# Optimization experiments

Measured on AMD Instinct MI355X. Metric: run time of the kernel, lower is better.

The kernel has to match this reference:

```python
import jax, jax.numpy as jnp
import numpy as np

IMAGE_SIZE = 224  # self.image_size; dims are all equal to this so postprocess is one bilinear resize
EPS = 1e-12      # F.normalize default eps


def setup_inputs() -> dict:
    key = jax.random.key(0)
    k1, k2 = jax.random.split(key)
    embeddings = jax.random.normal(k1, (2, 9, 256, 48, 48), dtype=jnp.float32)
    # binary class masks in {0,1}; channel 0 (background) is recomputed inside forward
    prompt_masks = jax.random.randint(k2, (2, 8, 4, 48, 48), 0, 2).astype(jnp.float32)
    dims = jnp.full((2, 1, 2), IMAGE_SIZE, dtype=jnp.int32)  # all original sizes == image_size
    return {"embeddings": embeddings, "prompt_masks": prompt_masks, "dims": dims}


def reference(embeddings, prompt_masks, dims):
    B, M, D, H, W = embeddings.shape
    HW = H * W
    q = embeddings[:, 0]            # (B, D, H, W)  query
    s = embeddings[:, 1:]           # (B, M-1, D, H, W)  supports
    # F.normalize: x / max(||x||, eps) along the feature dim
    qn = q / jnp.maximum(jnp.sqrt(jnp.sum(q * q, axis=1, keepdims=True)), EPS)
    sn = s / jnp.maximum(jnp.sqrt(jnp.sum(s * s, axis=2, keepdims=True)), EPS)

    q2 = qn.reshape(B, D, HW).transpose(0, 2, 1)              # (B, Q, D)
    s2 = sn.reshape(B, M - 1, D, HW).transpose(0, 1, 3, 2)    # (B, M1, K, D)
    sim = jnp.einsum('bqd,bmkd->bqmk', q2, s2)                # (B, Q, M1, K) cosine sims

    # nearest-resize of prompt masks to compare_size==(H,W) is identity here (same size)
    N = prompt_masks.shape[2]
    pm = prompt_masks.reshape(B, M - 1, N, HW)
    background = (pm[:, :, 1:, :].sum(axis=2) == 0).astype(sim.dtype)  # (B, M1, HW)
    pm = pm.at[:, :, 0, :].set(background)

    neg_inf = jnp.array(-jnp.inf, sim.dtype)
    logits = []
    for n in range(N):  # small fixed class count
        cm = pm[:, :, n, :][:, None]                 # (B, 1, M1, K) broadcast over Q
        masked = jnp.where(cm == 0, neg_inf, sim)    # (B, Q, M1, K)
        logits.append(masked.reshape(B, HW, -1).max(axis=-1))  # (B, Q)
    logits = jnp.stack(logits, axis=1).reshape(B, N, H, W)

    # postprocess_masks: bilinear to image_size; all original sizes == image_size so the
    # per-image second interpolate is identity and padding amounts are zero.
    out = jax.image.resize(logits, (B, N, IMAGE_SIZE, IMAGE_SIZE), method='bilinear')
    # masks[:,0][masks[:,0]==-inf] = 0  (no-op here, kept for faithfulness)
    out = out.at[:, 0].set(jnp.where(jnp.isneginf(out[:, 0]), 0.0, out[:, 0]))
    return out
```

## Files before the change

### kernel.cpp

```cpp
#include <hip/hip_runtime.h>
#include <hip/hip_bf16.h>
#include <math.h>

#define BB 2
#define MM 9
#define MS 8
#define DD 256
#define HW 2304
#define NCLS 4
#define OUTR 224

typedef float floatx4 __attribute__((ext_vector_type(4)));
typedef __bf16 bf16x8 __attribute__((ext_vector_type(8)));
typedef unsigned short ushortx8 __attribute__((ext_vector_type(8)));

__device__ __forceinline__ unsigned enc_f(float f) {
    unsigned u = __float_as_uint(f);
    return (u & 0x80000000u) ? ~u : (u | 0x80000000u);
}
__device__ __forceinline__ float dec_f(unsigned k) {
    unsigned u = (k & 0x80000000u) ? (k & 0x7FFFFFFFu) : ~k;
    return __uint_as_float(u);
}

__global__ __launch_bounds__(256) void knorm(const float* __restrict__ emb,
                                             __hip_bfloat16* __restrict__ outp,
                                             unsigned* __restrict__ enc_logits) {
    __shared__ float tile[256][33];
    __shared__ float psum[8][32];
    __shared__ float sscale[32];
    const int bm   = blockIdx.y;
    const int pix0 = blockIdx.x * 32;
    const int tid  = threadIdx.x;

    int flat = (blockIdx.y * gridDim.x + blockIdx.x) * 256 + tid;
    if (flat < BB * NCLS * HW) enc_logits[flat] = 0u;

    const float* src = emb + (size_t)bm * DD * HW + pix0;
    {
        const int dr = tid >> 3;
        const int p4 = (tid & 7) * 4;
#pragma unroll
        for (int r = 0; r < 8; ++r) {
            int d = r * 32 + dr;
            floatx4 v = *(const floatx4*)(src + (size_t)d * HW + p4);
            float* t = &tile[d][p4];
            t[0] = v[0]; t[1] = v[1]; t[2] = v[2]; t[3] = v[3];
        }
    }
    __syncthreads();
    {
        const int pc = tid & 31;
        const int dr = tid >> 5;
        float ss = 0.f;
#pragma unroll
        for (int s = 0; s < 32; ++s) {
            float v = tile[dr * 32 + s][pc];
            ss += v * v;
        }
        psum[dr][pc] = ss;
    }
    __syncthreads();
    if (tid < 32) {
        float t = 0.f;
#pragma unroll
        for (int c = 0; c < 8; ++c) t += psum[c][tid];
        sscale[tid] = 1.0f / fmaxf(sqrtf(t), 1e-12f);
    }
    __syncthreads();
    unsigned* dstu = (unsigned*)(outp + (size_t)bm * HW * DD + (size_t)pix0 * DD);
    const int d2 = tid & 127;
    const int ph = tid >> 7;
#pragma unroll
    for (int it = 0; it < 16; ++it) {
        int p = it * 2 + ph;
        float sc = sscale[p];
        float v0 = tile[2 * d2][p] * sc;
        float v1 = tile[2 * d2 + 1][p] * sc;
        unsigned pack = ((unsigned)__bfloat16_as_ushort(__float2bfloat16(v1)) << 16) |
                        (unsigned)__bfloat16_as_ushort(__float2bfloat16(v0));
        dstu[(size_t)p * 128 + d2] = pack;
    }
}

__device__ __forceinline__ void gld16(const unsigned short* g, unsigned short* l) {
    __builtin_amdgcn_global_load_lds((__attribute__((address_space(1))) void*)g,
                                     (__attribute__((address_space(3))) void*)l, 16, 0, 0);
}

#define BK 32
#define REDSTRIDE 132
#define SMEM_BYTES 33792

__global__ __launch_bounds__(256, 4) void kgemm(const unsigned short* __restrict__ normed,
                                                const float* __restrict__ pm,
                                                unsigned* __restrict__ enc_logits) {
    __shared__ __attribute__((aligned(16))) unsigned char smem[SMEM_BYTES];
    unsigned short* const S0 = (unsigned short*)smem;
    float* red = (float*)smem;

    const int ct = blockIdx.x;
    const int rt = blockIdx.y;
    const int b  = blockIdx.z;
    const int m  = ct / 18;
    const int kt = ct % 18;

    const int tid  = threadIdx.x;
    const int lane = tid & 63;
    const int wave = tid >> 6;
    const int wr = wave >> 1, wc = wave & 1;
    const int lrow = lane & 15;
    const int quad = lane >> 4;

    const unsigned short* A  = normed + (size_t)(b * MM) * (HW * DD) + (size_t)(rt * 128) * DD;
    const unsigned short* Bp = normed + (size_t)(b * MM + 1 + m) * (HW * DD) + (size_t)(kt * 128) * DD;

    const float* pmB = pm + (size_t)(b * MS + m) * NCLS * HW;
    int mj[4];
#pragma unroll
    for (int j = 0; j < 4; ++j) {
        int kp = kt * 128 + wc * 64 + j * 16 + lrow;
        float p1 = pmB[HW + kp], p2 = pmB[2 * HW + kp], p3 = pmB[3 * HW + kp];
        mj[j] = ((p1 + p2 + p3 == 0.0f) ? 1 : 0) | (p1 != 0.0f ? 2 : 0) |
                (p2 != 0.0f ? 4 : 0) | (p3 != 0.0f ? 8 : 0);
    }

    const int srq  = lane >> 2;
    const int scol = ((lane & 3) ^ ((srq >> 1) & 3)) * 8;
    const unsigned short* gA = A  + (size_t)(wave * 32 + srq) * DD + scol;
    const unsigned short* gB = Bp + (size_t)(wave * 32 + srq) * DD + scol;

    floatx4 zero = {0.f, 0.f, 0.f, 0.f};
    floatx4 acc[4][4];
#pragma unroll
    for (int i = 0; i < 4; ++i)
#pragma unroll
        for (int j = 0; j < 4; ++j) acc[i][j] = zero;

#pragma unroll
    for (int q = 0; q < 2; ++q) {
        gld16(gA + (size_t)(q * 16) * DD, S0 +        (wave * 2 + q) * 512);
        gld16(gB + (size_t)(q * 16) * DD, S0 + 4096 + (wave * 2 + q) * 512);
    }
    __syncthreads();

    const int pc8 = (quad ^ ((lrow >> 1) & 3)) * 8;

#pragma unroll
    for (int t = 0; t < DD / BK; ++t) {
        const int cb = t & 1;
        unsigned short* const Ac = S0 + cb * 8192;
        unsigned short* const Bc = Ac + 4096;
        if (t < DD / BK - 1) {
            unsigned short* const An = S0 + (cb ^ 1) * 8192;
#pragma unroll
            for (int q = 0; q < 2; ++q) {
                gld16(gA + (size_t)(q * 16) * DD + (t + 1) * BK, An +        (wave * 2 + q) * 512);
                gld16(gB + (size_t)(q * 16) * DD + (t + 1) * BK, An + 4096 + (wave * 2 + q) * 512);
            }
        }
        bf16x8 af[4], bfr[4];
#pragma unroll
        for (int i = 0; i < 4; ++i) {
            int ar = wr * 64 + i * 16 + lrow;
            int br = wc * 64 + i * 16 + lrow;
            af[i]  = __builtin_bit_cast(bf16x8, *(const ushortx8*)(Ac + ar * 32 + pc8));
            bfr[i] = __builtin_bit_cast(bf16x8, *(const ushortx8*)(Bc + br * 32 + pc8));
        }
#pragma unroll
        for (int i = 0; i < 4; ++i)
#pragma unroll
            for (int j = 0; j < 4; ++j)
                acc[i][j] = __builtin_amdgcn_mfma_f32_16x16x32_bf16(af[i], bfr[j], acc[i][j], 0, 0, 0);
        __syncthreads();
    }

    const int col32 = wc * 16 + lrow;

#pragma unroll
    for (int p = 0; p < 2; ++p) {
        if (p) __syncthreads();
        bool bit[2][4];
#pragma unroll
        for (int nn = 0; nn < 2; ++nn) {
            int n = p * 2 + nn;
#pragma unroll
            for (int j = 0; j < 4; ++j) bit[nn][j] = (mj[j] >> n) & 1;
        }
#pragma unroll
        for (int nn = 0; nn < 2; ++nn) {
#pragma unroll
            for (int i = 0; i < 4; ++i) {
                floatx4 o;
#pragma unroll
                for (int r = 0; r < 4; ++r) {
                    float t0 = bit[nn][0] ? acc[i][0][r] : -INFINITY;
                    float t1 = bit[nn][1] ? acc[i][1][r] : -INFINITY;
                    float t2 = bit[nn][2] ? acc[i][2][r] : -INFINITY;
                    float t3 = bit[nn][3] ? acc[i][3][r] : -INFINITY;
                    o[r] = fmaxf(fmaxf(t0, t1), fmaxf(t2, t3));
                }
                int rowbase = wr * 64 + i * 16 + quad * 4;
                *(floatx4*)(red + ((size_t)(nn * 32 + col32)) * REDSTRIDE + rowbase) = o;
            }
        }
        __syncthreads();
        {
            int nn  = tid >> 7;
            int row = tid & 127;
            float v = -INFINITY;
#pragma unroll
            for (int c = 0; c < 32; ++c)
                v = fmaxf(v, red[((size_t)(nn * 32 + c)) * REDSTRIDE + row]);
            int n = p * 2 + nn;
            atomicMax(enc_logits + ((size_t)b * NCLS + n) * HW + rt * 128 + row, enc_f(v));
        }
    }
}

__global__ __launch_bounds__(256) void kresize(const unsigned* __restrict__ enc_logits,
                                               float* __restrict__ out) {
    int idx = blockIdx.x * 256 + threadIdx.x;
    if (idx >= BB * NCLS * OUTR * OUTR) return;
    int ox = idx % OUTR;
    int oy = (idx / OUTR) % OUTR;
    int bn = idx / (OUTR * OUTR);
    const unsigned* src = enc_logits + (size_t)bn * HW;
    const float inv = 48.0f / 224.0f;
    float sx = (ox + 0.5f) * inv - 0.5f;
    float sy = (oy + 0.5f) * inv - 0.5f;
    int x0 = (int)floorf(sx); float fx = sx - x0;
    int y0 = (int)floorf(sy); float fy = sy - y0;
    int x0c = min(max(x0, 0), 47), x1c = min(max(x0 + 1, 0), 47);
    int y0c = min(max(y0, 0), 47), y1c = min(max(y0 + 1, 0), 47);
    float v00 = dec_f(src[y0c * 48 + x0c]), v01 = dec_f(src[y0c * 48 + x1c]);
    float v10 = dec_f(src[y1c * 48 + x0c]), v11 = dec_f(src[y1c * 48 + x1c]);
    float v = (1.f - fy) * ((1.f - fx) * v00 + fx * v01) + fy * ((1.f - fx) * v10 + fx * v11);
    if ((bn & 3) == 0 && v == -INFINITY) v = 0.f;
    out[idx] = v;
}

extern "C" void kernel_launch(void* const* d_in, const int* in_sizes, int n_in,
                              void* d_out, int out_size, void* d_ws, size_t ws_size,
                              hipStream_t stream) {
    const float* emb = (const float*)d_in[0];
    const float* pm  = (const float*)d_in[1];
    float* out = (float*)d_out;

    char* ws = (char*)d_ws;
    const size_t normed_bytes = (size_t)BB * MM * HW * DD * 2;
    __hip_bfloat16* normed = (__hip_bfloat16*)(ws);
    unsigned*       enc    = (unsigned*)(ws + normed_bytes);

    knorm<<<dim3(HW / 32, BB * MM), 256, 0, stream>>>(emb, normed, enc);
    kgemm<<<dim3(144, 18, BB), 256, 0, stream>>>((const unsigned short*)normed, pm, enc);
    kresize<<<(BB * NCLS * OUTR * OUTR + 255) / 256, 256, 0, stream>>>(enc, out);
}
```

Before: 144.3 us.

## Replace atomicMax logit reduction with per-tile partials and a separate reduction kernel

The GEMM kernel previously combined per-column-tile maxima with encoded-float atomicMax into a zero-initialised buffer. Each column tile now writes its own partial maxima to a workspace slab, and a new reduction kernel takes the max over the 144 tiles before the resize. This removes atomic contention, the order-preserving encode/decode and the init done in the norm kernel. In exchange it adds about 10 MB of partial writes and reads plus an extra kernel launch.

```diff
diff --git a/kernel.cpp b/kernel.cpp
--- a/kernel.cpp
+++ b/kernel.cpp
@@ -9,32 +9,20 @@
 #define HW 2304
 #define NCLS 4
 #define OUTR 224
+#define NCT 144
 
 typedef float floatx4 __attribute__((ext_vector_type(4)));
 typedef __bf16 bf16x8 __attribute__((ext_vector_type(8)));
 typedef unsigned short ushortx8 __attribute__((ext_vector_type(8)));
 
-__device__ __forceinline__ unsigned enc_f(float f) {
-    unsigned u = __float_as_uint(f);
-    return (u & 0x80000000u) ? ~u : (u | 0x80000000u);
-}
-__device__ __forceinline__ float dec_f(unsigned k) {
-    unsigned u = (k & 0x80000000u) ? (k & 0x7FFFFFFFu) : ~k;
-    return __uint_as_float(u);
-}
-
 __global__ __launch_bounds__(256) void knorm(const float* __restrict__ emb,
-                                             __hip_bfloat16* __restrict__ outp,
-                                             unsigned* __restrict__ enc_logits) {
+                                             __hip_bfloat16* __restrict__ outp) {
     __shared__ float tile[256][33];
     __shared__ float psum[8][32];
     __shared__ float sscale[32];
     const int bm   = blockIdx.y;
     const int pix0 = blockIdx.x * 32;
     const int tid  = threadIdx.x;
-
-    int flat = (blockIdx.y * gridDim.x + blockIdx.x) * 256 + tid;
-    if (flat < BB * NCLS * HW) enc_logits[flat] = 0u;
 
     const float* src = emb + (size_t)bm * DD * HW + pix0;
     {
@@ -94,7 +82,7 @@
 
 __global__ __launch_bounds__(256, 4) void kgemm(const unsigned short* __restrict__ normed,
                                                 const float* __restrict__ pm,
-                                                unsigned* __restrict__ enc_logits) {
+                                                float* __restrict__ partial) {
     __shared__ __attribute__((aligned(16))) unsigned char smem[SMEM_BYTES];
     unsigned short* const S0 = (unsigned short*)smem;
     float* red = (float*)smem;
@@ -213,19 +201,32 @@
             for (int c = 0; c < 32; ++c)
                 v = fmaxf(v, red[((size_t)(nn * 32 + c)) * REDSTRIDE + row]);
             int n = p * 2 + nn;
-            atomicMax(enc_logits + ((size_t)b * NCLS + n) * HW + rt * 128 + row, enc_f(v));
-        }
-    }
-}
-
-__global__ __launch_bounds__(256) void kresize(const unsigned* __restrict__ enc_logits,
+            partial[((size_t)ct * BB + b) * (NCLS * HW) + (size_t)n * HW + rt * 128 + row] = v;
+        }
+    }
+}
+
+__global__ __launch_bounds__(256) void kred(const float* __restrict__ partial,
+                                            float* __restrict__ logits) {
+    int idx = blockIdx.x * 256 + threadIdx.x;
+    int b    = idx / (NCLS * HW);
+    int rest = idx % (NCLS * HW);
+    const float* p = partial + (size_t)b * (NCLS * HW) + rest;
+    float v = -INFINITY;
+#pragma unroll 8
+    for (int ct = 0; ct < NCT; ++ct)
+        v = fmaxf(v, p[(size_t)ct * (BB * NCLS * HW)]);
+    logits[idx] = v;
+}
+
+__global__ __launch_bounds__(256) void kresize(const float* __restrict__ logits,
                                                float* __restrict__ out) {
     int idx = blockIdx.x * 256 + threadIdx.x;
     if (idx >= BB * NCLS * OUTR * OUTR) return;
     int ox = idx % OUTR;
     int oy = (idx / OUTR) % OUTR;
     int bn = idx / (OUTR * OUTR);
-    const unsigned* src = enc_logits + (size_t)bn * HW;
+    const float* src = logits + (size_t)bn * HW;
     const float inv = 48.0f / 224.0f;
     float sx = (ox + 0.5f) * inv - 0.5f;
     float sy = (oy + 0.5f) * inv - 0.5f;
@@ -233,8 +234,8 @@
     int y0 = (int)floorf(sy); float fy = sy - y0;
     int x0c = min(max(x0, 0), 47), x1c = min(max(x0 + 1, 0), 47);
     int y0c = min(max(y0, 0), 47), y1c = min(max(y0 + 1, 0), 47);
-    float v00 = dec_f(src[y0c * 48 + x0c]), v01 = dec_f(src[y0c * 48 + x1c]);
-    float v10 = dec_f(src[y1c * 48 + x0c]), v11 = dec_f(src[y1c * 48 + x1c]);
+    float v00 = src[y0c * 48 + x0c], v01 = src[y0c * 48 + x1c];
+    float v10 = src[y1c * 48 + x0c], v11 = src[y1c * 48 + x1c];
     float v = (1.f - fy) * ((1.f - fx) * v00 + fx * v01) + fy * ((1.f - fx) * v10 + fx * v11);
     if ((bn & 3) == 0 && v == -INFINITY) v = 0.f;
     out[idx] = v;
@@ -248,11 +249,14 @@
     float* out = (float*)d_out;
 
     char* ws = (char*)d_ws;
-    const size_t normed_bytes = (size_t)BB * MM * HW * DD * 2;
-    __hip_bfloat16* normed = (__hip_bfloat16*)(ws);
-    unsigned*       enc    = (unsigned*)(ws + normed_bytes);
-
-    knorm<<<dim3(HW / 32, BB * MM), 256, 0, stream>>>(emb, normed, enc);
-    kgemm<<<dim3(144, 18, BB), 256, 0, stream>>>((const unsigned short*)normed, pm, enc);
-    kresize<<<(BB * NCLS * OUTR * OUTR + 255) / 256, 256, 0, stream>>>(enc, out);
-}
+    const size_t normed_bytes  = (size_t)BB * MM * HW * DD * 2;
+    const size_t partial_bytes = (size_t)NCT * BB * NCLS * HW * 4;
+    __hip_bfloat16* normed  = (__hip_bfloat16*)(ws);
+    float*          partial = (float*)(ws + normed_bytes);
+    float*          logits  = (float*)(ws + normed_bytes + partial_bytes);
+
+    knorm<<<dim3(HW / 32, BB * MM), 256, 0, stream>>>(emb, normed);
+    kgemm<<<dim3(NCT, 18, BB), 256, 0, stream>>>((const unsigned short*)normed, pm, partial);
+    kred<<<(BB * NCLS * HW) / 256, 256, 0, stream>>>(partial, logits);
+    kresize<<<(BB * NCLS * OUTR * OUTR + 255) / 256, 256, 0, stream>>>(logits, out);
+}
```

Result: slower. 174.7 us (+21.1%).

## Load A fragments directly from global memory, stage only B through LDS

Applied to the files above, without the earlier changes.

The GEMM main loop no longer stages the query (A) tile through shared memory. Each wave reads its A fragments straight from global memory into registers, and only the support (B) tile is double-buffered in LDS. This halves LDS traffic and staging work per iteration, and A rows are reused across the K loop through the cache. The trade-off is that A global loads now sit on the MFMA critical path with no prefetch, and wave pairs sharing rows load the same A data redundantly.

```diff
diff --git a/kernel.cpp b/kernel.cpp
--- a/kernel.cpp
+++ b/kernel.cpp
@@ -127,8 +127,9 @@
 
     const int srq  = lane >> 2;
     const int scol = ((lane & 3) ^ ((srq >> 1) & 3)) * 8;
-    const unsigned short* gA = A  + (size_t)(wave * 32 + srq) * DD + scol;
-    const unsigned short* gB = Bp + (size_t)(wave * 32 + srq) * DD + scol;
+    const unsigned short* gB = Bp + (size_t)srq * DD + scol;
+
+    const unsigned short* gAf = A + (size_t)(wr * 64 + lrow) * DD + quad * 8;
 
     floatx4 zero = {0.f, 0.f, 0.f, 0.f};
     floatx4 acc[4][4];
@@ -137,11 +138,16 @@
 #pragma unroll
         for (int j = 0; j < 4; ++j) acc[i][j] = zero;
 
-#pragma unroll
-    for (int q = 0; q < 2; ++q) {
-        gld16(gA + (size_t)(q * 16) * DD, S0 +        (wave * 2 + q) * 512);
-        gld16(gB + (size_t)(q * 16) * DD, S0 + 4096 + (wave * 2 + q) * 512);
-    }
+#define STAGEB(bufN, tS) do {                                                  \
+        _Pragma("unroll")                                                      \
+        for (int q_ = 0; q_ < 2; ++q_) {                                       \
+            int g_ = wave * 2 + q_;                                            \
+            gld16(gB + (size_t)(g_ * 16) * DD + (tS) * BK,                     \
+                  S0 + (bufN) * 4096 + g_ * 512);                              \
+        }                                                                      \
+    } while (0)
+
+    STAGEB(0, 0);
     __syncthreads();
 
     const int pc8 = (quad ^ ((lrow >> 1) & 3)) * 8;
@@ -149,22 +155,14 @@
 #pragma unroll
     for (int t = 0; t < DD / BK; ++t) {
         const int cb = t & 1;
-        unsigned short* const Ac = S0 + cb * 8192;
-        unsigned short* const Bc = Ac + 4096;
-        if (t < DD / BK - 1) {
-            unsigned short* const An = S0 + (cb ^ 1) * 8192;
-#pragma unroll
-            for (int q = 0; q < 2; ++q) {
-                gld16(gA + (size_t)(q * 16) * DD + (t + 1) * BK, An +        (wave * 2 + q) * 512);
-                gld16(gB + (size_t)(q * 16) * DD + (t + 1) * BK, An + 4096 + (wave * 2 + q) * 512);
-            }
-        }
+        if (t < DD / BK - 1) STAGEB(cb ^ 1, t + 1);
+        const unsigned short* Bc = S0 + cb * 4096;
         bf16x8 af[4], bfr[4];
 #pragma unroll
         for (int i = 0; i < 4; ++i) {
-            int ar = wr * 64 + i * 16 + lrow;
+            af[i]  = __builtin_bit_cast(bf16x8,
+                         *(const ushortx8*)(gAf + (size_t)(i * 16) * DD + t * BK));
             int br = wc * 64 + i * 16 + lrow;
-            af[i]  = __builtin_bit_cast(bf16x8, *(const ushortx8*)(Ac + ar * 32 + pc8));
             bfr[i] = __builtin_bit_cast(bf16x8, *(const ushortx8*)(Bc + br * 32 + pc8));
         }
 #pragma unroll
@@ -174,6 +172,7 @@
                 acc[i][j] = __builtin_amdgcn_mfma_f32_16x16x32_bf16(af[i], bfr[j], acc[i][j], 0, 0, 0);
         __syncthreads();
     }
+#undef STAGEB
 
     const int col32 = wc * 16 + lrow;
 
```

Result: slower. 213.0 us (+47.6%).

## Swap MFMA operands so masked max reduces in registers and shuffles

Applied to the files above, without the earlier changes.

Swaps the A/B operands of the MFMA so each lane's accumulator registers run along the support (K) dimension instead of the query rows. The masked max over K can then be done in registers plus two cross-lane shuffles, replacing the large shared-memory reduction buffer and its two-pass barrier loop. Mask codes are computed once per block into a small LDS byte array instead of per lane. The aim is less LDS traffic and fewer barriers in the epilogue, at the cost of more register-held max state (16 floats) and per-element select/max work in registers.

```diff
diff --git a/kernel.cpp b/kernel.cpp
--- a/kernel.cpp
+++ b/kernel.cpp
@@ -89,15 +89,15 @@
 }
 
 #define BK 32
-#define REDSTRIDE 132
-#define SMEM_BYTES 33792
+#define SMEM_BYTES 32896
 
 __global__ __launch_bounds__(256, 4) void kgemm(const unsigned short* __restrict__ normed,
                                                 const float* __restrict__ pm,
                                                 unsigned* __restrict__ enc_logits) {
     __shared__ __attribute__((aligned(16))) unsigned char smem[SMEM_BYTES];
     unsigned short* const S0 = (unsigned short*)smem;
-    float* red = (float*)smem;
+    unsigned char* const mclds = smem + 32768;
+    float* const fin = (float*)smem;
 
     const int ct = blockIdx.x;
     const int rt = blockIdx.y;
@@ -116,13 +116,12 @@
     const unsigned short* Bp = normed + (size_t)(b * MM + 1 + m) * (HW * DD) + (size_t)(kt * 128) * DD;
 
     const float* pmB = pm + (size_t)(b * MS + m) * NCLS * HW;
-    int mj[4];
-#pragma unroll
-    for (int j = 0; j < 4; ++j) {
-        int kp = kt * 128 + wc * 64 + j * 16 + lrow;
-        float p1 = pmB[HW + kp], p2 = pmB[2 * HW + kp], p3 = pmB[3 * HW + kp];
-        mj[j] = ((p1 + p2 + p3 == 0.0f) ? 1 : 0) | (p1 != 0.0f ? 2 : 0) |
-                (p2 != 0.0f ? 4 : 0) | (p3 != 0.0f ? 8 : 0);
+    if (tid < 128) {
+        int s = kt * 128 + tid;
+        float p1 = pmB[HW + s], p2 = pmB[2 * HW + s], p3 = pmB[3 * HW + s];
+        unsigned code = ((p1 + p2 + p3 == 0.0f) ? 1u : 0u) | (p1 != 0.0f ? 2u : 0u) |
+                        (p2 != 0.0f ? 4u : 0u) | (p3 != 0.0f ? 8u : 0u);
+        mclds[tid] = (unsigned char)code;
     }
 
     const int srq  = lane >> 2;
@@ -171,49 +170,59 @@
         for (int i = 0; i < 4; ++i)
 #pragma unroll
             for (int j = 0; j < 4; ++j)
-                acc[i][j] = __builtin_amdgcn_mfma_f32_16x16x32_bf16(af[i], bfr[j], acc[i][j], 0, 0, 0);
+                acc[i][j] = __builtin_amdgcn_mfma_f32_16x16x32_bf16(bfr[j], af[i], acc[i][j], 0, 0, 0);
         __syncthreads();
     }
 
-    const int col32 = wc * 16 + lrow;
-
-#pragma unroll
-    for (int p = 0; p < 2; ++p) {
-        if (p) __syncthreads();
-        bool bit[2][4];
-#pragma unroll
-        for (int nn = 0; nn < 2; ++nn) {
-            int n = p * 2 + nn;
-#pragma unroll
-            for (int j = 0; j < 4; ++j) bit[nn][j] = (mj[j] >> n) & 1;
-        }
-#pragma unroll
-        for (int nn = 0; nn < 2; ++nn) {
-#pragma unroll
-            for (int i = 0; i < 4; ++i) {
-                floatx4 o;
-#pragma unroll
-                for (int r = 0; r < 4; ++r) {
-                    float t0 = bit[nn][0] ? acc[i][0][r] : -INFINITY;
-                    float t1 = bit[nn][1] ? acc[i][1][r] : -INFINITY;
-                    float t2 = bit[nn][2] ? acc[i][2][r] : -INFINITY;
-                    float t3 = bit[nn][3] ? acc[i][3][r] : -INFINITY;
-                    o[r] = fmaxf(fmaxf(t0, t1), fmaxf(t2, t3));
+    float vmax[4][4];
+#pragma unroll
+    for (int i = 0; i < 4; ++i)
+#pragma unroll
+        for (int n = 0; n < 4; ++n) vmax[i][n] = -INFINITY;
+
+#pragma unroll
+    for (int j = 0; j < 4; ++j) {
+        unsigned mcw = *(const unsigned*)(mclds + wc * 64 + j * 16 + quad * 4);
+#pragma unroll
+        for (int r = 0; r < 4; ++r) {
+            unsigned code = mcw >> (8 * r);
+#pragma unroll
+            for (int n = 0; n < 4; ++n) {
+                bool on = (code >> n) & 1;
+#pragma unroll
+                for (int i = 0; i < 4; ++i) {
+                    float tv = on ? acc[i][j][r] : -INFINITY;
+                    vmax[i][n] = fmaxf(vmax[i][n], tv);
                 }
-                int rowbase = wr * 64 + i * 16 + quad * 4;
-                *(floatx4*)(red + ((size_t)(nn * 32 + col32)) * REDSTRIDE + rowbase) = o;
             }
         }
-        __syncthreads();
-        {
-            int nn  = tid >> 7;
-            int row = tid & 127;
-            float v = -INFINITY;
-#pragma unroll
-            for (int c = 0; c < 32; ++c)
-                v = fmaxf(v, red[((size_t)(nn * 32 + c)) * REDSTRIDE + row]);
-            int n = p * 2 + nn;
-            atomicMax(enc_logits + ((size_t)b * NCLS + n) * HW + rt * 128 + row, enc_f(v));
+    }
+#pragma unroll
+    for (int i = 0; i < 4; ++i)
+#pragma unroll
+        for (int n = 0; n < 4; ++n) {
+            float v = vmax[i][n];
+            v = fmaxf(v, __shfl_xor(v, 16));
+            v = fmaxf(v, __shfl_xor(v, 32));
+            vmax[i][n] = v;
+        }
+    if (lane < 16) {
+#pragma unroll
+        for (int i = 0; i < 4; ++i) {
+            floatx4 o;
+#pragma unroll
+            for (int n = 0; n < 4; ++n) o[n] = vmax[i][n];
+            *(floatx4*)(fin + ((size_t)(wc * 128 + wr * 64 + i * 16 + lane)) * 4) = o;
+        }
+    }
+    __syncthreads();
+    if (tid < 128) {
+        floatx4 f0 = *(const floatx4*)(fin + (size_t)(0 * 128 + tid) * 4);
+        floatx4 f1 = *(const floatx4*)(fin + (size_t)(1 * 128 + tid) * 4);
+#pragma unroll
+        for (int n = 0; n < 4; ++n) {
+            float v = fmaxf(f0[n], f1[n]);
+            atomicMax(enc_logits + ((size_t)b * NCLS + n) * HW + rt * 128 + tid, enc_f(v));
         }
     }
 }
```

Result: slower. 150.6 us (+4.4%).
